# Optimization experiments

Measured on AMD Instinct MI355X. Metric: run time of the kernel, lower is better.

Reference implementation:

```python
import jax, jax.numpy as jnp
import numpy as np

N, E, D, H, F = 50000, 800000, 256, 4, 32
NEG_SLOPE = 0.2

def setup_inputs() -> dict:
    key = jax.random.key(0)
    ks = jax.random.split(key, 8)
    h = jax.random.normal(ks[0], (N, D), dtype=jnp.float32)
    W = jax.random.normal(ks[1], (D, H * F), dtype=jnp.float32) * (1.0 / np.sqrt(D))
    attn_l_w = jax.random.normal(ks[2], (F, 1), dtype=jnp.float32) * (1.0 / np.sqrt(F))
    attn_l_b = jnp.zeros((1,), dtype=jnp.float32)
    attn_r_w = jax.random.normal(ks[3], (F, 1), dtype=jnp.float32) * (1.0 / np.sqrt(F))
    attn_r_b = jnp.zeros((1,), dtype=jnp.float32)
    bias = jnp.zeros((H, F), dtype=jnp.float32)
    src = jax.random.randint(ks[4], (E,), 0, N, dtype=jnp.int32)
    dst = jax.random.randint(ks[5], (E,), 0, N, dtype=jnp.int32)
    return {"h": h, "W": W, "attn_l_w": attn_l_w, "attn_l_b": attn_l_b,
            "attn_r_w": attn_r_w, "attn_r_b": attn_r_b, "bias": bias,
            "src": src, "dst": dst}

def reference(h, W, attn_l_w, attn_l_b, attn_r_w, attn_r_b, bias, src, dst):
    # node projection: [N, D] @ [D, H*F] -> [N, H, F]
    hW = (h @ W).reshape(N, H, F)
    # per-node attention halves: Dense(1) over F -> [N, H, 1]
    el = jnp.einsum('nhf,fo->nho', hW, attn_l_w) + attn_l_b
    er = jnp.einsum('nhf,fo->nho', hW, attn_r_w) + attn_r_b
    # edge logits: src contributes er, dst contributes el -> [E, H, 1]
    e = er[src] + el[dst]
    e = jnp.where(e >= 0, e, NEG_SLOPE * e)  # leaky_relu
    # segment softmax over destination groups
    emax = jax.ops.segment_max(e, dst, num_segments=N)  # [N, H, 1]
    ee = jnp.exp(e - emax[dst])
    denom = jax.ops.segment_sum(ee, dst, num_segments=N)  # [N, H, 1]
    a = ee / denom[dst]  # [E, H, 1]
    # weighted message scatter-sum: [E, H, F] -> [N, H, F]
    m = hW[src] * a
    out = jax.ops.segment_sum(m, dst, num_segments=N) + bias
    return out
```

## Files before the change

### kernel.cpp

```cpp
#include <hip/hip_runtime.h>
#include <hip/hip_bf16.h>

#define N_NODES 50000
#define E_EDGES 800000
#define D_IN    256
#define H_HEADS 4
#define HF      128
#define NEG_SLOPE 0.2f
#define SCAN_BLOCKS ((N_NODES + 255) / 256)
#define PREP_BLOCKS 128
#define ZERO_BLOCKS SCAN_BLOCKS
#define GEMM_BLOCKS ((N_NODES + 63) / 64)

#define HIST_FAT_BLOCKS 625
#define HIST_STRIDE (HIST_FAT_BLOCKS * 256)

#define FILL_WINDOWS 8
#define FILL_WIN_NODES (N_NODES / FILL_WINDOWS)
#define FILL_EDGES_PER_SLICE 2048
#define FILL_SLICES ((E_EDGES + FILL_EDGES_PER_SLICE - 1) / FILL_EDGES_PER_SLICE)

typedef __attribute__((ext_vector_type(8))) short bf16x8;
typedef __attribute__((ext_vector_type(4))) float f32x4;

__device__ __forceinline__ float bf_lo(unsigned u) { return __uint_as_float(u << 16); }
__device__ __forceinline__ float bf_hi(unsigned u) { return __uint_as_float(u & 0xFFFF0000u); }

__global__ __launch_bounds__(256) void k_zero_prep(unsigned* __restrict__ cnt,
                                                   const float* __restrict__ W,
                                                   __hip_bfloat16* __restrict__ Wt) {
    const int b = blockIdx.x;
    if (b < ZERO_BLOCKS) {
        const int g = b * 256 + threadIdx.x;
        if (g < N_NODES) cnt[g] = 0u;
    } else {
        const int g = (b - ZERO_BLOCKS) * 256 + threadIdx.x;
        const int n = g >> 8;
        const int k = g & 255;
        Wt[n * D_IN + k] = __float2bfloat16(W[k * HF + n]);
    }
}

__global__ __launch_bounds__(256) void k_gemm_hist(const float* __restrict__ h,
                                                   const __hip_bfloat16* __restrict__ Wt,
                                                   const float* __restrict__ lw,
                                                   const float* __restrict__ lb,
                                                   const float* __restrict__ rw,
                                                   const float* __restrict__ rb,
                                                   __hip_bfloat16* __restrict__ hW,
                                                   float* __restrict__ el,
                                                   float* __restrict__ er,
                                                   const int* __restrict__ dst,
                                                   unsigned* __restrict__ cnt) {
    __shared__ __hip_bfloat16 As[64][72];
    __shared__ __hip_bfloat16 Bs[128][72];

    if (blockIdx.x >= GEMM_BLOCKS) {
        const int g0 = (blockIdx.x - GEMM_BLOCKS) * 256 + threadIdx.x;
        int d[5];
        #pragma unroll
        for (int i = 0; i < 5; ++i) d[i] = dst[g0 + i * HIST_STRIDE];
        #pragma unroll
        for (int i = 0; i < 5; ++i) atomicAdd(&cnt[d[i]], 1u);
        return;
    }

    const int t    = threadIdx.x;
    const int r0   = blockIdx.x * 64;
    const int wave = t >> 6;
    const int lane = t & 63;
    const int l16  = lane & 15;
    const int quad = lane >> 4;

    f32x4 acc[8] = {};

    for (int k0 = 0; k0 < D_IN; k0 += 64) {
        {
            const int row  = t >> 2;
            const int koff = (t & 3) * 16;
            const int n    = r0 + row;
            float v[16];
            if (n < N_NODES) {
                const float* p = h + (size_t)n * D_IN + k0 + koff;
                *(float4*)&v[0]  = ((const float4*)p)[0];
                *(float4*)&v[4]  = ((const float4*)p)[1];
                *(float4*)&v[8]  = ((const float4*)p)[2];
                *(float4*)&v[12] = ((const float4*)p)[3];
            } else {
                #pragma unroll
                for (int i = 0; i < 16; ++i) v[i] = 0.f;
            }
            __hip_bfloat16 b[16];
            #pragma unroll
            for (int i = 0; i < 16; ++i) b[i] = __float2bfloat16(v[i]);
            *(uint4*)&As[row][koff]     = ((uint4*)b)[0];
            *(uint4*)&As[row][koff + 8] = ((uint4*)b)[1];
        }
        {
            const int n    = t >> 1;
            const int koff = (t & 1) * 32;
            const uint4* p = (const uint4*)(Wt + n * D_IN + k0 + koff);
            uint4 b0 = p[0], b1 = p[1], b2 = p[2], b3 = p[3];
            uint4* q = (uint4*)&Bs[n][koff];
            q[0] = b0; q[1] = b1; q[2] = b2; q[3] = b3;
        }
        __syncthreads();

        #pragma unroll
        for (int ks = 0; ks < 2; ++ks) {
            const bf16x8 af = *(const bf16x8*)&As[wave * 16 + l16][ks * 32 + quad * 8];
            #pragma unroll
            for (int nt = 0; nt < 8; ++nt) {
                const bf16x8 bfg = *(const bf16x8*)&Bs[nt * 16 + l16][ks * 32 + quad * 8];
                acc[nt] = __builtin_amdgcn_mfma_f32_16x16x32_bf16(af, bfg, acc[nt], 0, 0, 0);
            }
        }
        __syncthreads();
    }

    const int mbase = r0 + wave * 16 + quad * 4;
    #pragma unroll
    for (int nt = 0; nt < 8; ++nt) {
        #pragma unroll
        for (int r = 0; r < 4; ++r) {
            const int m = mbase + r;
            if (m < N_NODES)
                hW[(size_t)m * HF + nt * 16 + l16] = __float2bfloat16(acc[nt][r]);
        }
    }

    const float lwv0 = lw[l16], lwv1 = lw[l16 + 16];
    const float rwv0 = rw[l16], rwv1 = rw[l16 + 16];
    const float lb0 = lb[0], rb0 = rb[0];
    #pragma unroll
    for (int r = 0; r < 4; ++r) {
        const int m = mbase + r;
        float el4[4], er4[4];
        #pragma unroll
        for (int hh = 0; hh < 4; ++hh) {
            float pl = acc[2 * hh][r] * lwv0 + acc[2 * hh + 1][r] * lwv1;
            float pr = acc[2 * hh][r] * rwv0 + acc[2 * hh + 1][r] * rwv1;
            #pragma unroll
            for (int o = 1; o < 16; o <<= 1) {
                pl += __shfl_xor(pl, o);
                pr += __shfl_xor(pr, o);
            }
            el4[hh] = pl + lb0;
            er4[hh] = pr + rb0;
        }
        if (l16 == 0 && m < N_NODES) {
            *(float4*)&el[m * H_HEADS] = make_float4(el4[0], el4[1], el4[2], el4[3]);
            *(float4*)&er[m * H_HEADS] = make_float4(er4[0], er4[1], er4[2], er4[3]);
        }
    }
}

__global__ __launch_bounds__(256) void k_scan(const unsigned* __restrict__ cnt,
                                              unsigned* __restrict__ off) {
    __shared__ unsigned s[256];
    const int t = threadIdx.x;
    const int b = blockIdx.x;
    const int base = b * 256;

    unsigned part = 0;
    #pragma unroll 4
    for (int i = t; i < base; i += 256) part += cnt[i];
    s[t] = part;
    __syncthreads();
    #pragma unroll
    for (int o = 128; o > 0; o >>= 1) {
        if (t < o) s[t] += s[t + o];
        __syncthreads();
    }
    const unsigned pre = s[0];
    __syncthreads();

    const int g = base + t;
    const unsigned x = (g < N_NODES) ? cnt[g] : 0u;
    s[t] = x;
    __syncthreads();
    unsigned inc = x;
    #pragma unroll
    for (int o = 1; o < 256; o <<= 1) {
        const unsigned v = (t >= o) ? s[t - o] : 0u;
        __syncthreads();
        inc += v;
        s[t] = inc;
        __syncthreads();
    }
    if (g < N_NODES) off[g] = pre + inc - x;
}

__global__ __launch_bounds__(256) void k_fill(const int* __restrict__ src,
                                              const int* __restrict__ dst,
                                              unsigned* __restrict__ off,
                                              unsigned* __restrict__ perm) {
    const int win   = blockIdx.x & 7;
    const int slice = blockIdx.x >> 3;
    const int base  = slice * FILL_EDGES_PER_SLICE + threadIdx.x;
    const int lo    = win * FILL_WIN_NODES;
    #pragma unroll
    for (int i = 0; i < 8; ++i) {
        const int g = base + i * 256;
        if (g < E_EDGES) {
            const int d = dst[g];
            if ((unsigned)(d - lo) < (unsigned)FILL_WIN_NODES) {
                const unsigned p = atomicAdd(&off[d], 1u);
                perm[p] = (unsigned)src[g];
            }
        }
    }
}

__global__ __launch_bounds__(256) void k_aggregate(const __hip_bfloat16* __restrict__ hW,
                                                   const float* __restrict__ el,
                                                   const float* __restrict__ er,
                                                   const unsigned* __restrict__ off_end,
                                                   const unsigned* __restrict__ perm,
                                                   const float* __restrict__ bias,
                                                   float* __restrict__ out) {
    const int wave = threadIdx.x >> 6;
    const int lane = threadIdx.x & 63;
    const int half = lane >> 5;
    const int l    = lane & 31;
    const int hh   = l >> 3;
    const int n    = blockIdx.x * 4 + wave;
    const unsigned beg = (n == 0) ? 0u : off_end[n - 1];
    const unsigned end = off_end[n];
    const float eld = el[(unsigned)n * H_HEADS + hh];
    const uint2* hW2 = (const uint2*)hW;

    float a0 = 0.f, a1 = 0.f, a2 = 0.f, a3 = 0.f, denom = 0.f;
    unsigned j = beg;
    for (; j + 8 <= end; j += 8) {
        const unsigned s0 = perm[j + half];
        const unsigned s1 = perm[j + 2 + half];
        const unsigned s2 = perm[j + 4 + half];
        const unsigned s3 = perm[j + 6 + half];
        const float er0 = er[s0 * H_HEADS + hh];
        const float er1 = er[s1 * H_HEADS + hh];
        const float er2 = er[s2 * H_HEADS + hh];
        const float er3 = er[s3 * H_HEADS + hh];
        const uint2 g0 = hW2[s0 * 32u + l];
        const uint2 g1 = hW2[s1 * 32u + l];
        const uint2 g2 = hW2[s2 * 32u + l];
        const uint2 g3 = hW2[s3 * 32u + l];
        float v0 = er0 + eld; v0 = (v0 >= 0.f) ? v0 : NEG_SLOPE * v0;
        float v1 = er1 + eld; v1 = (v1 >= 0.f) ? v1 : NEG_SLOPE * v1;
        float v2 = er2 + eld; v2 = (v2 >= 0.f) ? v2 : NEG_SLOPE * v2;
        float v3 = er3 + eld; v3 = (v3 >= 0.f) ? v3 : NEG_SLOPE * v3;
        const float p0 = __expf(v0);
        const float p1 = __expf(v1);
        const float p2 = __expf(v2);
        const float p3 = __expf(v3);
        denom += (p0 + p1) + (p2 + p3);
        a0 += p0 * bf_lo(g0.x) + p1 * bf_lo(g1.x) + p2 * bf_lo(g2.x) + p3 * bf_lo(g3.x);
        a1 += p0 * bf_hi(g0.x) + p1 * bf_hi(g1.x) + p2 * bf_hi(g2.x) + p3 * bf_hi(g3.x);
        a2 += p0 * bf_lo(g0.y) + p1 * bf_lo(g1.y) + p2 * bf_lo(g2.y) + p3 * bf_lo(g3.y);
        a3 += p0 * bf_hi(g0.y) + p1 * bf_hi(g1.y) + p2 * bf_hi(g2.y) + p3 * bf_hi(g3.y);
    }
    if (j + 4 <= end) {
        const unsigned s0 = perm[j + half];
        const unsigned s1 = perm[j + 2 + half];
        const float er0 = er[s0 * H_HEADS + hh];
        const float er1 = er[s1 * H_HEADS + hh];
        const uint2 g0 = hW2[s0 * 32u + l];
        const uint2 g1 = hW2[s1 * 32u + l];
        float v0 = er0 + eld; v0 = (v0 >= 0.f) ? v0 : NEG_SLOPE * v0;
        float v1 = er1 + eld; v1 = (v1 >= 0.f) ? v1 : NEG_SLOPE * v1;
        const float p0 = __expf(v0);
        const float p1 = __expf(v1);
        denom += p0 + p1;
        a0 += p0 * bf_lo(g0.x) + p1 * bf_lo(g1.x);
        a1 += p0 * bf_hi(g0.x) + p1 * bf_hi(g1.x);
        a2 += p0 * bf_lo(g0.y) + p1 * bf_lo(g1.y);
        a3 += p0 * bf_hi(g0.y) + p1 * bf_hi(g1.y);
        j += 4;
    }
    for (; j < end; j += 2) {
        const unsigned i = j + half;
        const bool ok = (i < end);
        const unsigned s = ok ? perm[i] : 0u;
        const float erv = er[s * H_HEADS + hh];
        const uint2 g = hW2[s * 32u + l];
        float v = erv + eld; v = (v >= 0.f) ? v : NEG_SLOPE * v;
        const float p = ok ? __expf(v) : 0.f;
        denom += p;
        a0 += p * bf_lo(g.x);
        a1 += p * bf_hi(g.x);
        a2 += p * bf_lo(g.y);
        a3 += p * bf_hi(g.y);
    }
    denom += __shfl_xor(denom, 32);
    a0 += __shfl_xor(a0, 32);
    a1 += __shfl_xor(a1, 32);
    a2 += __shfl_xor(a2, 32);
    a3 += __shfl_xor(a3, 32);
    if (half == 0) {
        const float inv = (end > beg) ? 1.f / denom : 0.f;
        const float4 bv = *(const float4*)&bias[l * 4];
        float4 o = make_float4(a0 * inv + bv.x, a1 * inv + bv.y,
                               a2 * inv + bv.z, a3 * inv + bv.w);
        *(float4*)&out[(unsigned)n * HF + l * 4] = o;
    }
}

extern "C" void kernel_launch(void* const* d_in, const int* in_sizes, int n_in,
                              void* d_out, int out_size, void* d_ws, size_t ws_size,
                              hipStream_t stream) {
    const float* h    = (const float*)d_in[0];
    const float* W    = (const float*)d_in[1];
    const float* lw   = (const float*)d_in[2];
    const float* lb   = (const float*)d_in[3];
    const float* rw   = (const float*)d_in[4];
    const float* rb   = (const float*)d_in[5];
    const float* bias = (const float*)d_in[6];
    const int*   src  = (const int*)d_in[7];
    const int*   dst  = (const int*)d_in[8];
    float* out = (float*)d_out;

    float*    ws   = (float*)d_ws;
    float*    el   = ws;
    float*    er   = ws + 200000;
    unsigned* cnt  = (unsigned*)(ws + 400000);
    unsigned* off  = (unsigned*)(ws + 450000);
    unsigned* perm = (unsigned*)(ws + 500000);
    __hip_bfloat16* Wt = (__hip_bfloat16*)(ws + 1300000);
    __hip_bfloat16* hW = (__hip_bfloat16*)(ws + 1320000);

    k_zero_prep<<<ZERO_BLOCKS + PREP_BLOCKS, 256, 0, stream>>>(cnt, W, Wt);
    k_gemm_hist<<<GEMM_BLOCKS + HIST_FAT_BLOCKS, 256, 0, stream>>>(
        h, Wt, lw, lb, rw, rb, hW, el, er, dst, cnt);
    k_scan<<<SCAN_BLOCKS, 256, 0, stream>>>(cnt, off);
    k_fill<<<FILL_SLICES * FILL_WINDOWS, 256, 0, stream>>>(src, dst, off, perm);
    k_aggregate<<<N_NODES / 4, 256, 0, stream>>>(hW, el, er, off, perm, bias, out);
}
```

Measured before the change: 226.5 us.

## Load GEMM MFMA operands directly from global memory, dropping LDS staging

The projection GEMM no longer stages the h and Wt tiles through shared memory with block barriers. Each lane now loads its A fragment straight from h, converts it to bf16 in registers, and reads B fragments directly from the small Wt matrix, which is expected to sit in cache. This removes the LDS writes, reads and __syncthreads, and frees shared memory for occupancy. The cost is more global and L2 traffic for Wt, since every wave re-reads the whole 128x256 matrix, plus less coalesced, strided accesses to h.

```diff
diff --git a/kernel.cpp b/kernel.cpp
--- a/kernel.cpp
+++ b/kernel.cpp
@@ -52,9 +52,6 @@
                                                    float* __restrict__ er,
                                                    const int* __restrict__ dst,
                                                    unsigned* __restrict__ cnt) {
-    __shared__ __hip_bfloat16 As[64][72];
-    __shared__ __hip_bfloat16 Bs[128][72];
-
     if (blockIdx.x >= GEMM_BLOCKS) {
         const int g0 = (blockIdx.x - GEMM_BLOCKS) * 256 + threadIdx.x;
         int d[5];
@@ -72,50 +69,41 @@
     const int l16  = lane & 15;
     const int quad = lane >> 4;
 
+    const int  arow = r0 + wave * 16 + l16;
+    const bool aok  = (arow < N_NODES);
+    const float* hrow = h + (size_t)arow * D_IN;
+
     f32x4 acc[8] = {};
 
+    #pragma unroll
     for (int k0 = 0; k0 < D_IN; k0 += 64) {
-        {
-            const int row  = t >> 2;
-            const int koff = (t & 3) * 16;
-            const int n    = r0 + row;
-            float v[16];
-            if (n < N_NODES) {
-                const float* p = h + (size_t)n * D_IN + k0 + koff;
-                *(float4*)&v[0]  = ((const float4*)p)[0];
-                *(float4*)&v[4]  = ((const float4*)p)[1];
-                *(float4*)&v[8]  = ((const float4*)p)[2];
-                *(float4*)&v[12] = ((const float4*)p)[3];
+        #pragma unroll
+        for (int ks = 0; ks < 2; ++ks) {
+            const int kc = k0 + ks * 32 + quad * 8;
+            bf16x8 af;
+            if (aok) {
+                const float4 f0 = *(const float4*)(hrow + kc);
+                const float4 f1 = *(const float4*)(hrow + kc + 4);
+                __hip_bfloat16 tb[8];
+                tb[0] = __float2bfloat16(f0.x);
+                tb[1] = __float2bfloat16(f0.y);
+                tb[2] = __float2bfloat16(f0.z);
+                tb[3] = __float2bfloat16(f0.w);
+                tb[4] = __float2bfloat16(f1.x);
+                tb[5] = __float2bfloat16(f1.y);
+                tb[6] = __float2bfloat16(f1.z);
+                tb[7] = __float2bfloat16(f1.w);
+                af = *(const bf16x8*)tb;
             } else {
-                #pragma unroll
-                for (int i = 0; i < 16; ++i) v[i] = 0.f;
+                af = bf16x8{0, 0, 0, 0, 0, 0, 0, 0};
             }
-            __hip_bfloat16 b[16];
-            #pragma unroll
-            for (int i = 0; i < 16; ++i) b[i] = __float2bfloat16(v[i]);
-            *(uint4*)&As[row][koff]     = ((uint4*)b)[0];
-            *(uint4*)&As[row][koff + 8] = ((uint4*)b)[1];
-        }
-        {
-            const int n    = t >> 1;
-            const int koff = (t & 1) * 32;
-            const uint4* p = (const uint4*)(Wt + n * D_IN + k0 + koff);
-            uint4 b0 = p[0], b1 = p[1], b2 = p[2], b3 = p[3];
-            uint4* q = (uint4*)&Bs[n][koff];
-            q[0] = b0; q[1] = b1; q[2] = b2; q[3] = b3;
-        }
-        __syncthreads();
-
-        #pragma unroll
-        for (int ks = 0; ks < 2; ++ks) {
-            const bf16x8 af = *(const bf16x8*)&As[wave * 16 + l16][ks * 32 + quad * 8];
             #pragma unroll
             for (int nt = 0; nt < 8; ++nt) {
-                const bf16x8 bfg = *(const bf16x8*)&Bs[nt * 16 + l16][ks * 32 + quad * 8];
+                const bf16x8 bfg =
+                    *(const bf16x8*)(Wt + (size_t)(nt * 16 + l16) * D_IN + kc);
                 acc[nt] = __builtin_amdgcn_mfma_f32_16x16x32_bf16(af, bfg, acc[nt], 0, 0, 0);
             }
         }
-        __syncthreads();
     }
 
     const int mbase = r0 + wave * 16 + quad * 4;
```

Result: slower. 245.0 us (+8.2%).
